# Kernel tuning notes

Hardware: AMD Instinct MI355X
Metric: run time of the kernel (lower is better)

Reference implementation:

```python
import jax, jax.numpy as jnp
import numpy as np

N_NODES = 100000
N_EDGES = 1600000
IN_DIM = 128
FEAT_DIM = 128
N_CLS = 40


def _glorot(key, shape):
    fan_in = shape[1]
    bound = 1.0 / np.sqrt(fan_in)
    return jax.random.uniform(key, shape, jnp.float32, -bound, bound)


def setup_inputs() -> dict:
    key = jax.random.key(0)
    ks = jax.random.split(key, 12)
    x = jax.random.normal(ks[0], (N_NODES, IN_DIM), jnp.float32)
    edge_index = jax.random.randint(ks[1], (2, N_EDGES), 0, N_NODES, jnp.int64)
    edge_weight = jax.random.uniform(ks[2], (N_EDGES,), jnp.float32)
    # layer 1 (in=IN_DIM, out=FEAT_DIM)
    W1_l = _glorot(ks[3], (FEAT_DIM, IN_DIM))
    b1_l = jnp.zeros((FEAT_DIM,), jnp.float32)
    W1_r = _glorot(ks[4], (FEAT_DIM, IN_DIM))
    # layer 2 (in=FEAT_DIM, out=FEAT_DIM)
    W2_l = _glorot(ks[5], (FEAT_DIM, FEAT_DIM))
    b2_l = jnp.zeros((FEAT_DIM,), jnp.float32)
    W2_r = _glorot(ks[6], (FEAT_DIM, FEAT_DIM))
    # classifier
    Wc = _glorot(ks[7], (N_CLS, FEAT_DIM))
    bc = jnp.zeros((N_CLS,), jnp.float32)
    return {"x": x, "edge_index": edge_index, "edge_weight": edge_weight,
            "W1_l": W1_l, "b1_l": b1_l, "W1_r": W1_r,
            "W2_l": W2_l, "b2_l": b2_l, "W2_r": W2_r,
            "Wc": Wc, "bc": bc}


def _sage_conv(x, src, dst, W_l, b_l, W_r):
    # mean aggregation of neighbor features: mean_{j in N(i)} x_j
    msg = x[src]                                        # [E, F] gather
    agg = jax.ops.segment_sum(msg, dst, num_segments=N_NODES)  # [N, F]
    deg = jax.ops.segment_sum(jnp.ones((src.shape[0],), x.dtype), dst,
                              num_segments=N_NODES)     # [N]
    mean = agg / jnp.maximum(deg, 1.0)[:, None]         # isolated nodes -> 0
    out = mean @ W_l.T + b_l                            # lin_l
    out = out + x @ W_r.T                               # root (temp_weight)
    return out


def reference(x, edge_index, edge_weight, W1_l, b1_l, W1_r, W2_l, b2_l, W2_r, Wc, bc):
    src = edge_index[0]
    dst = edge_index[1]
    h = jax.nn.relu(_sage_conv(x, src, dst, W1_l, b1_l, W1_r))
    h = jax.nn.relu(_sage_conv(h, src, dst, W2_l, b2_l, W2_r))
    # dropout is identity in eval mode
    return h @ Wc.T + bc
```

## Files before the change

### kernel.cpp

```cpp
#include <hip/hip_runtime.h>

#define NN 100000
#define NE 1600000
#define FD 128
#define NC 40
#define NBK 782
#define HISTB 256
#define CONVB 512
#define PREPB 276
#define CHUNK (NE / HISTB)

typedef __attribute__((ext_vector_type(8))) short short8;
typedef __attribute__((ext_vector_type(4))) float f32x4;

#define WS_OFF      0u
#define WS_INVDEG   400384u
#define WS_CNT      800512u
#define WS_BTOT     1601280u
#define WS_BKO      1604480u
#define WS_WB       1607680u
#define WS_CSR      1880576u
#define WS_XB       8280576u
#define WS_MB       33880576u
#define WS_HB       59480576u

__device__ inline unsigned short bf16_rne(float v) {
    union { float f; unsigned u; } a; a.f = v;
    return (unsigned short)((a.u + 0x7FFFu + ((a.u >> 16) & 1u)) >> 16);
}

__device__ inline void cvt_split(float v, unsigned short& h, unsigned short& l) {
    union { float f; unsigned u; } a; a.f = v;
    unsigned rh = (a.u + 0x7FFFu + ((a.u >> 16) & 1u)) >> 16;
    h = (unsigned short)rh;
    union { unsigned u; float f; } b; b.u = rh << 16;
    float lo = v - b.f;
    union { float f; unsigned u; } c; c.f = lo;
    l = (unsigned short)((c.u + 0x7FFFu + ((c.u >> 16) & 1u)) >> 16);
}

__global__ __launch_bounds__(256) void k_p1(
        const int* __restrict__ ei, int* __restrict__ cnt,
        const float* __restrict__ x, unsigned short* __restrict__ xb,
        const float* __restrict__ W1l, const float* __restrict__ W1r,
        const float* __restrict__ W2l, const float* __restrict__ W2r,
        const float* __restrict__ Wc, unsigned short* __restrict__ wb) {
    if (blockIdx.x < CONVB) {
        int i = blockIdx.x * 256 + threadIdx.x;
        const int total = NN * FD / 8;
        for (int s = i; s < total; s += CONVB * 256) {
            float4 a = *reinterpret_cast<const float4*>(x + (size_t)s * 8);
            float4 b = *reinterpret_cast<const float4*>(x + (size_t)s * 8 + 4);
            short8 o;
            o[0] = (short)bf16_rne(a.x); o[1] = (short)bf16_rne(a.y);
            o[2] = (short)bf16_rne(a.z); o[3] = (short)bf16_rne(a.w);
            o[4] = (short)bf16_rne(b.x); o[5] = (short)bf16_rne(b.y);
            o[6] = (short)bf16_rne(b.z); o[7] = (short)bf16_rne(b.w);
            *reinterpret_cast<short8*>(xb + (size_t)s * 8) = o;
        }
    } else if (blockIdx.x < CONVB + HISTB) {
        __shared__ int hist[NBK];
        const int* dst = ei + NE;
        int blk = blockIdx.x - CONVB;
        for (int j = threadIdx.x; j < NBK; j += 256) hist[j] = 0;
        __syncthreads();
        int base = blk * CHUNK;
        for (int i = threadIdx.x; i < CHUNK; i += 256)
            atomicAdd(&hist[dst[base + i] >> 7], 1);
        __syncthreads();
        for (int j = threadIdx.x; j < NBK; j += 256)
            cnt[blk * NBK + j] = hist[j];
    } else {
        int i = (blockIdx.x - CONVB - HISTB) * 256 + threadIdx.x;
        if (i < 65536) {
            int m = i >> 14, e = i & 16383;
            const float* W = (m == 0) ? W1l : (m == 1) ? W1r : (m == 2) ? W2l : W2r;
            unsigned short h, l;
            cvt_split(W[e], h, l);
            wb[m * 32768 + e] = h;
            wb[m * 32768 + 16384 + e] = l;
        } else if (i < 65536 + NC * FD) {
            int j = i - 65536;
            wb[131072 + j] = bf16_rne(Wc[j]);
        }
    }
}

__global__ __launch_bounds__(256) void k_p2a(int* __restrict__ cnt,
                                             int* __restrict__ btot) {
    __shared__ int s[256];
    int b = blockIdx.x, t = threadIdx.x;
    int v = cnt[t * NBK + b];
    s[t] = v;
    __syncthreads();
    for (int d = 1; d < 256; d <<= 1) {
        int x = (t >= d) ? s[t - d] : 0;
        __syncthreads();
        s[t] += x;
        __syncthreads();
    }
    cnt[t * NBK + b] = s[t] - v;
    if (t == 255) btot[b] = s[255];
}

__global__ __launch_bounds__(256) void k_p3(const int* __restrict__ ei,
                                            const int* __restrict__ cnt,
                                            const int* __restrict__ btot,
                                            int* __restrict__ bko,
                                            unsigned* __restrict__ bval) {
    __shared__ int bko_s[NBK + 1];
    __shared__ int cur[NBK];
    __shared__ int s[256];
    int t = threadIdx.x;
    int base = t * 4;
    int v[4]; int tsum = 0;
#pragma unroll
    for (int j = 0; j < 4; ++j) {
        int idx = base + j;
        v[j] = (idx < NBK) ? btot[idx] : 0;
        tsum += v[j];
    }
    s[t] = tsum;
    __syncthreads();
    for (int d = 1; d < 256; d <<= 1) {
        int x = (t >= d) ? s[t - d] : 0;
        __syncthreads();
        s[t] += x;
        __syncthreads();
    }
    int p = s[t] - tsum;
#pragma unroll
    for (int j = 0; j < 4; ++j) {
        int idx = base + j;
        if (idx <= NBK) bko_s[idx] = p;
        p += v[j];
    }
    __syncthreads();
    int blk = blockIdx.x;
    if (blk == 0) {
        for (int j = t; j <= NBK; j += 256) bko[j] = bko_s[j];
    }
    for (int j = t; j < NBK; j += 256)
        cur[j] = bko_s[j] + cnt[blk * NBK + j];
    __syncthreads();
    int ebase = blk * CHUNK;
    const int* src = ei;
    const int* dst = ei + NE;
    for (int i = t; i < CHUNK; i += 256) {
        int sv = src[ebase + i];
        int d  = dst[ebase + i];
        int pos = atomicAdd(&cur[d >> 7], 1);
        bval[pos] = (unsigned)sv | ((unsigned)(d & 127) << 17);
    }
}

__global__ __launch_bounds__(256) void k_p4(const unsigned* __restrict__ bval,
                                            const int* __restrict__ bko,
                                            int* __restrict__ csr,
                                            int* __restrict__ off,
                                            float* __restrict__ invdeg) {
    __shared__ int hist[128], curk[128], sc[128];
    int b = blockIdx.x, tid = threadIdx.x;
    int s = bko[b], e = bko[b + 1];
    if (tid < 128) hist[tid] = 0;
    __syncthreads();
    for (int i = s + tid; i < e; i += 256)
        atomicAdd(&hist[bval[i] >> 17], 1);
    __syncthreads();
    if (tid < 128) sc[tid] = hist[tid];
    __syncthreads();
    for (int d = 1; d < 128; d <<= 1) {
        int x = (tid >= d && tid < 128) ? sc[tid - d] : 0;
        __syncthreads();
        if (tid < 128) sc[tid] += x;
        __syncthreads();
    }
    if (tid < 128) {
        int excl = sc[tid] - hist[tid];
        curk[tid] = excl;
        int node = b * 128 + tid;
        if (node < NN) {
            off[node] = s + excl;
            int dg = hist[tid];
            invdeg[node] = 1.0f / (float)(dg > 0 ? dg : 1);
        }
    }
    if (b == 0 && tid == 0) off[NN] = NE;
    __syncthreads();
    for (int i = s + tid; i < e; i += 256) {
        unsigned v = bval[i];
        int dl = v >> 17;
        int r = atomicAdd(&curk[dl], 1);
        csr[s + r] = (int)(v & 0x1FFFFu);
    }
}

__device__ inline void acc8(float* a, uint4 v) {
    a[0] += __uint_as_float(v.x << 16);
    a[1] += __uint_as_float(v.x & 0xFFFF0000u);
    a[2] += __uint_as_float(v.y << 16);
    a[3] += __uint_as_float(v.y & 0xFFFF0000u);
    a[4] += __uint_as_float(v.z << 16);
    a[5] += __uint_as_float(v.z & 0xFFFF0000u);
    a[6] += __uint_as_float(v.w << 16);
    a[7] += __uint_as_float(v.w & 0xFFFF0000u);
}

__global__ __launch_bounds__(256) void k_agg(const unsigned short* __restrict__ Xb,
                                             const int* __restrict__ off,
                                             const int* __restrict__ csr,
                                             const float* __restrict__ invdeg,
                                             unsigned short* __restrict__ Mb) {
    int wid = (blockIdx.x * 256 + threadIdx.x) >> 6;
    int lane = threadIdx.x & 63;
    if (wid >= NN) return;
    const int g  = lane >> 4;
    const int fc = lane & 15;
    const unsigned short* Xl = Xb + fc * 8;
    int s0 = off[wid], s1 = off[wid + 1];
    float a[8] = {};
    int e = s0;
    if (e + 15 < s1) {
        uint4 p0 = *reinterpret_cast<const uint4*>(Xl + ((size_t)csr[e + g]      << 7));
        uint4 p1 = *reinterpret_cast<const uint4*>(Xl + ((size_t)csr[e + 4 + g]  << 7));
        uint4 p2 = *reinterpret_cast<const uint4*>(Xl + ((size_t)csr[e + 8 + g]  << 7));
        uint4 p3 = *reinterpret_cast<const uint4*>(Xl + ((size_t)csr[e + 12 + g] << 7));
        for (e += 16; e + 15 < s1; e += 16) {
            int j0 = csr[e + g];
            int j1 = csr[e + 4 + g];
            int j2 = csr[e + 8 + g];
            int j3 = csr[e + 12 + g];
            uint4 n0 = *reinterpret_cast<const uint4*>(Xl + ((size_t)j0 << 7));
            uint4 n1 = *reinterpret_cast<const uint4*>(Xl + ((size_t)j1 << 7));
            uint4 n2 = *reinterpret_cast<const uint4*>(Xl + ((size_t)j2 << 7));
            uint4 n3 = *reinterpret_cast<const uint4*>(Xl + ((size_t)j3 << 7));
            acc8(a, p0); acc8(a, p1); acc8(a, p2); acc8(a, p3);
            p0 = n0; p1 = n1; p2 = n2; p3 = n3;
        }
        acc8(a, p0); acc8(a, p1); acc8(a, p2); acc8(a, p3);
    }
    for (; e + 7 < s1; e += 8) {
        int r0 = csr[e + g];
        int r1 = csr[e + 4 + g];
        uint4 v0 = *reinterpret_cast<const uint4*>(Xl + ((size_t)r0 << 7));
        uint4 v1 = *reinterpret_cast<const uint4*>(Xl + ((size_t)r1 << 7));
        acc8(a, v0);
        acc8(a, v1);
    }
    for (; e < s1; e += 4) {
        int cnt = s1 - e;
        int r = csr[e + (g < cnt ? g : 0)];
        uint4 v = *reinterpret_cast<const uint4*>(Xl + ((size_t)r << 7));
        if (g < cnt) acc8(a, v);
    }
#pragma unroll
    for (int j = 0; j < 8; ++j) {
        a[j] += __shfl_xor(a[j], 32);
        a[j] += __shfl_xor(a[j], 16);
    }
    if (g == 0) {
        float w = invdeg[wid];
        uint4 o;
        o.x = (unsigned)bf16_rne(a[0] * w) | ((unsigned)bf16_rne(a[1] * w) << 16);
        o.y = (unsigned)bf16_rne(a[2] * w) | ((unsigned)bf16_rne(a[3] * w) << 16);
        o.z = (unsigned)bf16_rne(a[4] * w) | ((unsigned)bf16_rne(a[5] * w) << 16);
        o.w = (unsigned)bf16_rne(a[6] * w) | ((unsigned)bf16_rne(a[7] * w) << 16);
        *reinterpret_cast<uint4*>(Mb + (size_t)wid * FD + fc * 8) = o;
    }
}

template <bool FUSE>
__global__ __launch_bounds__(256, 3) void k_gemm(
        const unsigned short* __restrict__ M,
        const unsigned short* __restrict__ X,
        const unsigned short* __restrict__ Wl,
        const unsigned short* __restrict__ Wr,
        const float* __restrict__ bias,
        const unsigned short* __restrict__ Wcb,
        const float* __restrict__ bc,
        unsigned short* outb, float* outf) {
    __shared__ __align__(16) unsigned short pool[FUSE ? 21504 : 12800];
    unsigned short* Ah = pool;
    unsigned short* Bh = pool + 2560;
    unsigned short* Bl = pool + 7680;

    const int tid = threadIdx.x;
    const int wave = tid >> 6;
    const int lane = tid & 63;
    const int wm = wave & 1;
    const int wn = wave >> 1;
    const int nb = blockIdx.x * 64;
    const int l15 = lane & 15;
    const int kb = lane >> 4;

    f32x4 acc[2][4] = {};

    for (int c = 0; c < 8; ++c) {
        const unsigned short* A = (c < 4) ? M : X;
        const unsigned short* W = (c < 4) ? Wl : Wr;
        const int kc = (c & 3) * 32;
        __syncthreads();
        {
            int row = tid >> 2, seg = tid & 3;
            int gn = nb + row;
            short8 v = {};
            if (gn < NN)
                v = *reinterpret_cast<const short8*>(A + (size_t)gn * FD + kc + seg * 8);
            *reinterpret_cast<short8*>(&Ah[row * 40 + seg * 8]) = v;
        }
#pragma unroll
        for (int r = 0; r < 2; ++r) {
            int slot = tid + 256 * r;
            int o = slot >> 2, seg = slot & 3;
            short8 vh = *reinterpret_cast<const short8*>(W + o * FD + kc + seg * 8);
            short8 vl = *reinterpret_cast<const short8*>(W + 16384 + o * FD + kc + seg * 8);
            *reinterpret_cast<short8*>(&Bh[o * 40 + seg * 8]) = vh;
            *reinterpret_cast<short8*>(&Bl[o * 40 + seg * 8]) = vl;
        }
        __syncthreads();
        short8 a[2], b_h[4], b_l[4];
#pragma unroll
        for (int mt = 0; mt < 2; ++mt) {
            int row = wm * 32 + mt * 16 + l15;
            a[mt] = *reinterpret_cast<const short8*>(&Ah[row * 40 + kb * 8]);
        }
#pragma unroll
        for (int nt = 0; nt < 4; ++nt) {
            int o = wn * 64 + nt * 16 + l15;
            b_h[nt] = *reinterpret_cast<const short8*>(&Bh[o * 40 + kb * 8]);
            b_l[nt] = *reinterpret_cast<const short8*>(&Bl[o * 40 + kb * 8]);
        }
#pragma unroll
        for (int mt = 0; mt < 2; ++mt)
#pragma unroll
            for (int nt = 0; nt < 4; ++nt) {
                acc[mt][nt] = __builtin_amdgcn_mfma_f32_16x16x32_bf16(a[mt], b_h[nt], acc[mt][nt], 0, 0, 0);
                acc[mt][nt] = __builtin_amdgcn_mfma_f32_16x16x32_bf16(a[mt], b_l[nt], acc[mt][nt], 0, 0, 0);
            }
    }

    float bz[4];
#pragma unroll
    for (int nt = 0; nt < 4; ++nt) bz[nt] = bias[wn * 64 + nt * 16 + l15];

    if (!FUSE) {
#pragma unroll
        for (int mt = 0; mt < 2; ++mt) {
            int gn0 = nb + wm * 32 + mt * 16 + kb * 4;
#pragma unroll
            for (int r = 0; r < 4; ++r) {
                int gn = gn0 + r;
                if (gn < NN) {
#pragma unroll
                    for (int nt = 0; nt < 4; ++nt) {
                        float v = fmaxf(acc[mt][nt][r] + bz[nt], 0.f);
                        outb[(size_t)gn * FD + wn * 64 + nt * 16 + l15] = bf16_rne(v);
                    }
                }
            }
        }
    } else {
        unsigned short* Hs  = pool + 12800;
        unsigned short* Wcs = pool;
        __syncthreads();
#pragma unroll
        for (int r = 0; r < 3; ++r) {
            int slot = tid + 256 * r;
            if (slot < 640) {
                int row = slot >> 4, seg = slot & 15;
                *reinterpret_cast<short8*>(&Wcs[row * 136 + seg * 8]) =
                    *reinterpret_cast<const short8*>(Wcb + row * FD + seg * 8);
            }
        }
#pragma unroll
        for (int mt = 0; mt < 2; ++mt) {
            int row0 = wm * 32 + mt * 16 + kb * 4;
#pragma unroll
            for (int r = 0; r < 4; ++r) {
#pragma unroll
                for (int nt = 0; nt < 4; ++nt) {
                    float v = fmaxf(acc[mt][nt][r] + bz[nt], 0.f);
                    Hs[(row0 + r) * 136 + wn * 64 + nt * 16 + l15] = bf16_rne(v);
                }
            }
        }
        __syncthreads();
        f32x4 c2[3] = {};
#pragma unroll
        for (int kk = 0; kk < 4; ++kk) {
            short8 af = *reinterpret_cast<const short8*>(
                &Hs[(wave * 16 + l15) * 136 + kk * 32 + kb * 8]);
#pragma unroll
            for (int t = 0; t < 3; ++t) {
                short8 bf = *reinterpret_cast<const short8*>(
                    &Wcs[(t * 16 + l15) * 136 + kk * 32 + kb * 8]);
                c2[t] = __builtin_amdgcn_mfma_f32_16x16x32_bf16(af, bf, c2[t], 0, 0, 0);
            }
        }
#pragma unroll
        for (int t = 0; t < 3; ++t) {
            int cls = t * 16 + l15;
            if (cls < NC) {
#pragma unroll
                for (int r = 0; r < 4; ++r) {
                    int gn = nb + wave * 16 + kb * 4 + r;
                    if (gn < NN)
                        outf[(size_t)gn * NC + cls] = c2[t][r] + bc[cls];
                }
            }
        }
    }
}

extern "C" void kernel_launch(void* const* d_in, const int* in_sizes, int n_in,
                              void* d_out, int out_size, void* d_ws, size_t ws_size,
                              hipStream_t stream) {
    const float* x   = (const float*)d_in[0];
    const int*   ei  = (const int*)d_in[1];
    const float* W1l = (const float*)d_in[3];
    const float* b1l = (const float*)d_in[4];
    const float* W1r = (const float*)d_in[5];
    const float* W2l = (const float*)d_in[6];
    const float* b2l = (const float*)d_in[7];
    const float* W2r = (const float*)d_in[8];
    const float* Wc  = (const float*)d_in[9];
    const float* bc  = (const float*)d_in[10];
    float* out = (float*)d_out;

    char* ws = (char*)d_ws;
    int*   off    = (int*)(ws + WS_OFF);
    float* invdeg = (float*)(ws + WS_INVDEG);
    int*   cnt    = (int*)(ws + WS_CNT);
    int*   btot   = (int*)(ws + WS_BTOT);
    int*   bko    = (int*)(ws + WS_BKO);
    unsigned short* wb = (unsigned short*)(ws + WS_WB);
    int*   csr    = (int*)(ws + WS_CSR);
    unsigned short* xb = (unsigned short*)(ws + WS_XB);
    unsigned short* mb = (unsigned short*)(ws + WS_MB);
    unsigned short* hb = (unsigned short*)(ws + WS_HB);
    unsigned* bval = (unsigned*)(ws + WS_HB);

    k_p1<<<CONVB + HISTB + PREPB, 256, 0, stream>>>(ei, cnt, x, xb,
                                                    W1l, W1r, W2l, W2r, Wc, wb);
    k_p2a<<<NBK, 256, 0, stream>>>(cnt, btot);
    k_p3<<<HISTB, 256, 0, stream>>>(ei, cnt, btot, bko, bval);
    k_p4<<<NBK, 256, 0, stream>>>(bval, bko, csr, off, invdeg);

    const int GG = (NN + 63) / 64;

    k_agg<<<(NN + 3) / 4, 256, 0, stream>>>(xb, off, csr, invdeg, mb);
    k_gemm<false><<<GG, 256, 0, stream>>>(mb, xb, wb, wb + 32768, b1l,
                                          nullptr, nullptr, hb, nullptr);
    k_agg<<<(NN + 3) / 4, 256, 0, stream>>>(hb, off, csr, invdeg, mb);
    k_gemm<true><<<GG, 256, 0, stream>>>(mb, hb, wb + 65536, wb + 98304, b2l,
                                         wb + 131072, bc, nullptr, out);
}
```

Baseline: 233.6 us.

## Retile SAGE GEMM to 128-row blocks with A fragments loaded directly from global

Each GEMM block now covers 128 nodes instead of 64, and each wave owns 32 rows across all 128 output columns. A operands are read straight from global memory into registers, so the A shared-memory staging is gone. Weight tiles loaded into LDS are therefore reused across twice as many rows, which halves redundant weight traffic and the block count. In exchange each thread holds twice as many accumulators, adding register pressure that can reduce occupancy under launch_bounds(256,3), and the fused classifier epilogue needs a larger LDS buffer.

```diff
diff --git a/kernel.cpp b/kernel.cpp
--- a/kernel.cpp
+++ b/kernel.cpp
@@ -279,35 +279,32 @@
         const unsigned short* __restrict__ Wcb,
         const float* __restrict__ bc,
         unsigned short* outb, float* outf) {
-    __shared__ __align__(16) unsigned short pool[FUSE ? 21504 : 12800];
-    unsigned short* Ah = pool;
-    unsigned short* Bh = pool + 2560;
-    unsigned short* Bl = pool + 7680;
+    __shared__ __align__(16) unsigned short pool[FUSE ? 22848 : 10240];
+    unsigned short* Bh = pool;
+    unsigned short* Bl = pool + 5120;
 
     const int tid = threadIdx.x;
     const int wave = tid >> 6;
     const int lane = tid & 63;
-    const int wm = wave & 1;
-    const int wn = wave >> 1;
-    const int nb = blockIdx.x * 64;
+    const int nb = blockIdx.x * 128;
     const int l15 = lane & 15;
     const int kb = lane >> 4;
 
-    f32x4 acc[2][4] = {};
+    f32x4 acc[2][8] = {};
 
     for (int c = 0; c < 8; ++c) {
         const unsigned short* A = (c < 4) ? M : X;
         const unsigned short* W = (c < 4) ? Wl : Wr;
         const int kc = (c & 3) * 32;
-        __syncthreads();
-        {
-            int row = tid >> 2, seg = tid & 3;
-            int gn = nb + row;
-            short8 v = {};
-            if (gn < NN)
-                v = *reinterpret_cast<const short8*>(A + (size_t)gn * FD + kc + seg * 8);
-            *reinterpret_cast<short8*>(&Ah[row * 40 + seg * 8]) = v;
-        }
+        short8 a[2];
+#pragma unroll
+        for (int mt = 0; mt < 2; ++mt) {
+            int gn = nb + wave * 32 + mt * 16 + l15;
+            a[mt] = (gn < NN)
+                ? *reinterpret_cast<const short8*>(A + (size_t)gn * FD + kc + kb * 8)
+                : short8{};
+        }
+        __syncthreads();
 #pragma unroll
         for (int r = 0; r < 2; ++r) {
             int slot = tid + 256 * r;
@@ -318,50 +315,42 @@
             *reinterpret_cast<short8*>(&Bl[o * 40 + seg * 8]) = vl;
         }
         __syncthreads();
-        short8 a[2], b_h[4], b_l[4];
+#pragma unroll
+        for (int nt = 0; nt < 8; ++nt) {
+            int o = nt * 16 + l15;
+            short8 b_h = *reinterpret_cast<const short8*>(&Bh[o * 40 + kb * 8]);
+            short8 b_l = *reinterpret_cast<const short8*>(&Bl[o * 40 + kb * 8]);
+#pragma unroll
+            for (int mt = 0; mt < 2; ++mt) {
+                acc[mt][nt] = __builtin_amdgcn_mfma_f32_16x16x32_bf16(a[mt], b_h, acc[mt][nt], 0, 0, 0);
+                acc[mt][nt] = __builtin_amdgcn_mfma_f32_16x16x32_bf16(a[mt], b_l, acc[mt][nt], 0, 0, 0);
+            }
+        }
+    }
+
+    float bz[8];
+#pragma unroll
+    for (int nt = 0; nt < 8; ++nt) bz[nt] = bias[nt * 16 + l15];
+
+    if (!FUSE) {
 #pragma unroll
         for (int mt = 0; mt < 2; ++mt) {
-            int row = wm * 32 + mt * 16 + l15;
-            a[mt] = *reinterpret_cast<const short8*>(&Ah[row * 40 + kb * 8]);
-        }
-#pragma unroll
-        for (int nt = 0; nt < 4; ++nt) {
-            int o = wn * 64 + nt * 16 + l15;
-            b_h[nt] = *reinterpret_cast<const short8*>(&Bh[o * 40 + kb * 8]);
-            b_l[nt] = *reinterpret_cast<const short8*>(&Bl[o * 40 + kb * 8]);
-        }
-#pragma unroll
-        for (int mt = 0; mt < 2; ++mt)
-#pragma unroll
-            for (int nt = 0; nt < 4; ++nt) {
-                acc[mt][nt] = __builtin_amdgcn_mfma_f32_16x16x32_bf16(a[mt], b_h[nt], acc[mt][nt], 0, 0, 0);
-                acc[mt][nt] = __builtin_amdgcn_mfma_f32_16x16x32_bf16(a[mt], b_l[nt], acc[mt][nt], 0, 0, 0);
-            }
-    }
-
-    float bz[4];
-#pragma unroll
-    for (int nt = 0; nt < 4; ++nt) bz[nt] = bias[wn * 64 + nt * 16 + l15];
-
-    if (!FUSE) {
-#pragma unroll
-        for (int mt = 0; mt < 2; ++mt) {
-            int gn0 = nb + wm * 32 + mt * 16 + kb * 4;
+            int gn0 = nb + wave * 32 + mt * 16 + kb * 4;
 #pragma unroll
             for (int r = 0; r < 4; ++r) {
                 int gn = gn0 + r;
                 if (gn < NN) {
 #pragma unroll
-                    for (int nt = 0; nt < 4; ++nt) {
+                    for (int nt = 0; nt < 8; ++nt) {
                         float v = fmaxf(acc[mt][nt][r] + bz[nt], 0.f);
-                        outb[(size_t)gn * FD + wn * 64 + nt * 16 + l15] = bf16_rne(v);
+                        outb[(size_t)gn * FD + nt * 16 + l15] = bf16_rne(v);
                     }
                 }
             }
         }
     } else {
-        unsigned short* Hs  = pool + 12800;
-        unsigned short* Wcs = pool;
+        unsigned short* Hs  = pool;
+        unsigned short* Wcs = pool + 17408;
         __syncthreads();
 #pragma unroll
         for (int r = 0; r < 3; ++r) {
@@ -374,38 +363,44 @@
         }
 #pragma unroll
         for (int mt = 0; mt < 2; ++mt) {
-            int row0 = wm * 32 + mt * 16 + kb * 4;
+            int row0 = wave * 32 + mt * 16 + kb * 4;
 #pragma unroll
             for (int r = 0; r < 4; ++r) {
 #pragma unroll
-                for (int nt = 0; nt < 4; ++nt) {
+                for (int nt = 0; nt < 8; ++nt) {
                     float v = fmaxf(acc[mt][nt][r] + bz[nt], 0.f);
-                    Hs[(row0 + r) * 136 + wn * 64 + nt * 16 + l15] = bf16_rne(v);
+                    Hs[(row0 + r) * 136 + nt * 16 + l15] = bf16_rne(v);
                 }
             }
         }
         __syncthreads();
-        f32x4 c2[3] = {};
+        f32x4 c2[2][3] = {};
 #pragma unroll
         for (int kk = 0; kk < 4; ++kk) {
-            short8 af = *reinterpret_cast<const short8*>(
-                &Hs[(wave * 16 + l15) * 136 + kk * 32 + kb * 8]);
+#pragma unroll
+            for (int rt = 0; rt < 2; ++rt) {
+                short8 af = *reinterpret_cast<const short8*>(
+                    &Hs[(wave * 32 + rt * 16 + l15) * 136 + kk * 32 + kb * 8]);
+#pragma unroll
+                for (int t = 0; t < 3; ++t) {
+                    short8 bf = *reinterpret_cast<const short8*>(
+                        &Wcs[(t * 16 + l15) * 136 + kk * 32 + kb * 8]);
+                    c2[rt][t] = __builtin_amdgcn_mfma_f32_16x16x32_bf16(af, bf, c2[rt][t], 0, 0, 0);
+                }
+            }
+        }
+#pragma unroll
+        for (int rt = 0; rt < 2; ++rt) {
 #pragma unroll
             for (int t = 0; t < 3; ++t) {
-                short8 bf = *reinterpret_cast<const short8*>(
-                    &Wcs[(t * 16 + l15) * 136 + kk * 32 + kb * 8]);
-                c2[t] = __builtin_amdgcn_mfma_f32_16x16x32_bf16(af, bf, c2[t], 0, 0, 0);
-            }
-        }
-#pragma unroll
-        for (int t = 0; t < 3; ++t) {
-            int cls = t * 16 + l15;
-            if (cls < NC) {
-#pragma unroll
-                for (int r = 0; r < 4; ++r) {
-                    int gn = nb + wave * 16 + kb * 4 + r;
-                    if (gn < NN)
-                        outf[(size_t)gn * NC + cls] = c2[t][r] + bc[cls];
+                int cls = t * 16 + l15;
+                if (cls < NC) {
+#pragma unroll
+                    for (int r = 0; r < 4; ++r) {
+                        int gn = nb + wave * 32 + rt * 16 + kb * 4 + r;
+                        if (gn < NN)
+                            outf[(size_t)gn * NC + cls] = c2[rt][t][r] + bc[cls];
+                    }
                 }
             }
         }
@@ -446,7 +441,7 @@
     k_p3<<<HISTB, 256, 0, stream>>>(ei, cnt, btot, bko, bval);
     k_p4<<<NBK, 256, 0, stream>>>(bval, bko, csr, off, invdeg);
 
-    const int GG = (NN + 63) / 64;
+    const int GG = (NN + 127) / 128;
 
     k_agg<<<(NN + 3) / 4, 256, 0, stream>>>(xb, off, csr, invdeg, mb);
     k_gemm<false><<<GG, 256, 0, stream>>>(mb, xb, wb, wb + 32768, b1l,
```

After: 235.8 us. Within noise of the previous version (+0.9%).
